# Kernel tuning notes

Measured on AMD Instinct MI355X. Metric: run time of the kernel, lower is better.

The kernel has to match this reference:

```python
import jax, jax.numpy as jnp
import numpy as np

I, O, H, M, N = 64, 64, 512, 64, 128  # input, output, controller hidden, content bits, addresses
B, S = 32, 256
EPS = 1e-8
R_SZ = M + 6          # read head: key(M) + beta(1) + gate(1) + shift(3) + gamma(1)
W_SZ = 3 * M + 6      # write head: read params + erase(M) + add(M)


def _split_head(p, with_erase_add):
    k = jnp.tanh(p[:, :M])
    beta = jax.nn.softplus(p[:, M:M + 1])
    g = jax.nn.sigmoid(p[:, M + 1:M + 2])
    s = jax.nn.softmax(p[:, M + 2:M + 5], axis=-1)
    gamma = 1.0 + jax.nn.softplus(p[:, M + 5:M + 6])
    if with_erase_add:
        e = jax.nn.sigmoid(p[:, M + 6:2 * M + 6])
        a = jnp.tanh(p[:, 2 * M + 6:3 * M + 6])
        return k, beta, g, s, gamma, e, a
    return k, beta, g, s, gamma


def _address(k, beta, g, s, gamma, w_prev, mem):
    # k:[B,M] beta,g,gamma:[B,1] s:[B,3] w_prev:[B,N] mem:[B,N,M]
    knorm = jnp.linalg.norm(k, axis=-1, keepdims=True)   # [B,1]
    mnorm = jnp.linalg.norm(mem, axis=-1)                # [B,N]
    sim = jnp.einsum('bm,bnm->bn', k, mem) / (knorm * mnorm + EPS)
    wc = jax.nn.softmax(beta * sim, axis=-1)             # content addressing
    wg = g * wc + (1.0 - g) * w_prev                     # interpolation gate
    # circular convolution with shifts {-1, 0, +1}
    rolled = jnp.stack([jnp.roll(wg, o, axis=-1) for o in (-1, 0, 1)], axis=-1)  # [B,N,3]
    ws = jnp.einsum('bnt,bt->bn', rolled, s)
    wp = jnp.power(jnp.maximum(ws, 1e-12), gamma)        # sharpening
    return wp / jnp.sum(wp, axis=-1, keepdims=True)


def setup_inputs() -> dict:
    key = jax.random.key(0)
    ks = jax.random.split(key, 5)
    sc = 0.05
    ctrl_in = I + M + H  # external input + read vector + recurrent hidden
    return {
        'inputs': jax.random.normal(ks[0], (B, S, I), jnp.float32),
        'W_lstm': jax.random.normal(ks[1], (ctrl_in, 4 * H), jnp.float32) * sc,
        'b_lstm': jnp.zeros((4 * H,), jnp.float32),
        'W_int': jax.random.normal(ks[2], (H, R_SZ + W_SZ), jnp.float32) * sc,
        'b_int': jnp.zeros((R_SZ + W_SZ,), jnp.float32),
        'W_out': jax.random.normal(ks[3], (H + M, O), jnp.float32) * sc,
        'b_out': jnp.zeros((O,), jnp.float32),
    }


def reference(inputs, W_lstm, b_lstm, W_int, b_int, W_out, b_out):
    Bsz = inputs.shape[0]
    mem0 = jnp.full((Bsz, N, M), 0.01, jnp.float32)
    w0 = jnp.zeros((Bsz, N), jnp.float32).at[:, 0].set(1.0)
    h0 = jnp.zeros((Bsz, H), jnp.float32)
    c0 = jnp.zeros((Bsz, H), jnp.float32)
    r0 = jnp.full((Bsz, M), 0.01, jnp.float32)

    def step(carry, x_t):
        h, c, w_r, w_w, mem, r = carry
        # LSTM controller over [input, read vector]
        z = jnp.concatenate([x_t, r, h], axis=-1) @ W_lstm + b_lstm
        i_g, f_g, g_g, o_g = jnp.split(z, 4, axis=-1)
        c = jax.nn.sigmoid(f_g) * c + jax.nn.sigmoid(i_g) * jnp.tanh(g_g)
        h = jax.nn.sigmoid(o_g) * jnp.tanh(c)
        # interface parameters
        p = h @ W_int + b_int
        rk, rb, rg, rs, rgam = _split_head(p[:, :R_SZ], False)
        wk, wb, wg_, ws_, wgam, e, a = _split_head(p[:, R_SZ:], True)
        # write (erase then add), then read from updated memory
        w_w = _address(wk, wb, wg_, ws_, wgam, w_w, mem)
        mem = mem * (1.0 - w_w[:, :, None] * e[:, None, :]) + w_w[:, :, None] * a[:, None, :]
        w_r = _address(rk, rb, rg, rs, rgam, w_r, mem)
        r = jnp.einsum('bn,bnm->bm', w_r, mem)
        out = jnp.concatenate([h, r], axis=-1) @ W_out + b_out
        return (h, c, w_r, w_w, mem, r), out

    xs = jnp.swapaxes(inputs, 0, 1)  # [S,B,I]
    _, outs = jax.lax.scan(step, (h0, c0, w0, w0, mem0, r0), xs)
    return jnp.swapaxes(outs, 0, 1)  # [B,S,O]
```

## Files before the change

kernel.cpp:

```cpp
#include <hip/hip_runtime.h>
#include <hip/hip_fp16.h>
#include <math.h>

#define NI 64
#define NO 64
#define NH 512
#define NM 64
#define NN 128
#define NB 32
#define NS 256
#define ZD 2048
#define PD 268
#define NG 128
#define GBLK 160
#define TPB 512
#define UPB 4
#define ST 580
#define RS_ST 68

__device__ __forceinline__ float fexp(float x){ return __expf(x); }
__device__ __forceinline__ float sigm(float x){ return 1.0f/(1.0f+__expf(-x)); }
__device__ __forceinline__ float ftanh(float x){
  float e = __expf(2.f*x);
  return (x > 10.f) ? 1.f : (x < -10.f) ? -1.f : (e - 1.f)/(e + 1.f);
}
__device__ __forceinline__ float softplus_(float x){
  return (x > 15.f) ? x : __logf(1.f + __expf(x));
}
__device__ __forceinline__ float fpow_(float x, float g){
  return __expf(g*__logf(x));
}

typedef _Float16 h2_t __attribute__((ext_vector_type(2)));
#if defined(__has_builtin)
#if __has_builtin(__builtin_amdgcn_fdot2)
#define HAS_FDOT2 1
#endif
#endif
__device__ __forceinline__ float fdot2_(unsigned int w, unsigned int h, float acc){
#ifdef HAS_FDOT2
  return __builtin_amdgcn_fdot2(__builtin_bit_cast(h2_t, w),
                                __builtin_bit_cast(h2_t, h), acc, false);
#else
  float w0 = __half2float(__builtin_bit_cast(__half, (unsigned short)(w      )));
  float w1 = __half2float(__builtin_bit_cast(__half, (unsigned short)(w >> 16)));
  float h0 = __half2float(__builtin_bit_cast(__half, (unsigned short)(h      )));
  float h1 = __half2float(__builtin_bit_cast(__half, (unsigned short)(h >> 16)));
  return fmaf(w1, h1, fmaf(w0, h0, acc));
#endif
}

__device__ __forceinline__ float cloadf(const float* p){
  return __hip_atomic_load(p, __ATOMIC_RELAXED, __HIP_MEMORY_SCOPE_SYSTEM);
}
__device__ __forceinline__ void cstoref(float* p, float v){
  __hip_atomic_store(p, v, __ATOMIC_RELAXED, __HIP_MEMORY_SCOPE_SYSTEM);
}
__device__ __forceinline__ float2 cloadf2(const float* p){
  unsigned long long u = __hip_atomic_load((const unsigned long long*)p,
                                           __ATOMIC_RELAXED, __HIP_MEMORY_SCOPE_SYSTEM);
  return __builtin_bit_cast(float2, u);
}
__device__ __forceinline__ unsigned long long cload8(const void* p){
  return __hip_atomic_load((const unsigned long long*)p,
                           __ATOMIC_RELAXED, __HIP_MEMORY_SCOPE_SYSTEM);
}
__device__ __forceinline__ void cstore8(void* p, unsigned long long v){
  __hip_atomic_store((unsigned long long*)p, v,
                     __ATOMIC_RELAXED, __HIP_MEMORY_SCOPE_SYSTEM);
}
__device__ __forceinline__ int cloadi(const int* p){
  return __hip_atomic_load(p, __ATOMIC_RELAXED, __HIP_MEMORY_SCOPE_SYSTEM);
}
__device__ __forceinline__ void cstorei(int* p, int v){
  __hip_atomic_store(p, v, __ATOMIC_RELAXED, __HIP_MEMORY_SCOPE_SYSTEM);
}
__device__ __forceinline__ void caddi(int* p){
  __hip_atomic_fetch_add(p, 1, __ATOMIC_RELAXED, __HIP_MEMORY_SCOPE_SYSTEM);
}
__device__ __forceinline__ void cstoreh(unsigned short* p, unsigned short v){
  __hip_atomic_store(p, v, __ATOMIC_RELAXED, __HIP_MEMORY_SCOPE_SYSTEM);
}

__device__ __forceinline__ unsigned long long packh4(float a, float b, float c, float d){
  unsigned short u0 = __builtin_bit_cast(unsigned short, __float2half(a));
  unsigned short u1 = __builtin_bit_cast(unsigned short, __float2half(b));
  unsigned short u2 = __builtin_bit_cast(unsigned short, __float2half(c));
  unsigned short u3 = __builtin_bit_cast(unsigned short, __float2half(d));
  return (unsigned long long)u0 | ((unsigned long long)u1 << 16)
       | ((unsigned long long)u2 << 32) | ((unsigned long long)u3 << 48);
}
__device__ __forceinline__ void unpackh4(unsigned long long v, float* o){
  o[0] = __half2float(__builtin_bit_cast(__half, (unsigned short)(v      )));
  o[1] = __half2float(__builtin_bit_cast(__half, (unsigned short)(v >> 16)));
  o[2] = __half2float(__builtin_bit_cast(__half, (unsigned short)(v >> 32)));
  o[3] = __half2float(__builtin_bit_cast(__half, (unsigned short)(v >> 48)));
}

__device__ __forceinline__ void postFlag(int* flags, int idx, int era){
  __syncthreads();
  if (threadIdx.x == 0) cstorei(&flags[idx*16], era);
}
__device__ __forceinline__ void waitAll32(const int* flags, int era){
  if (threadIdx.x < 32) {
    while (cloadi(&flags[(int)threadIdx.x*16]) < era)
      __builtin_amdgcn_s_sleep(1);
  }
  __syncthreads();
}
__device__ __forceinline__ void postCnt(int* c){
  __syncthreads();
  if (threadIdx.x == 0) caddi(c);
}
__device__ __forceinline__ void waitCnt(const int* c, int target){
  if (threadIdx.x == 0) {
    while (cloadi(c) < target) __builtin_amdgcn_s_sleep(2);
  }
  __syncthreads();
}

struct P1S { float inT[NB*ST]; float zpart[4*16*32]; float rs[NB*RS_ST]; float hx[4*33]; };
struct P3S { float h[NH]; unsigned long long h16[128]; float pp[544]; float p[PD+4];
             float rk[NM], wk[NM], e[NM], a[NM];
             float sim[NN]; float red[8*64]; float r[NM]; };
union  USH { P1S p1; P3S p3; };

__device__ void address_head(int t, const float* __restrict__ ks,
                             const float* __restrict__ scal,
                             float* __restrict__ w_arr,
                             const float* __restrict__ mem_s,
                             float* __restrict__ sim_s)
{
  {
    int n = t >> 2, sub = t & 3;
    int cn = (n & 7) << 2;
    float dot = 0.f, sq = 0.f;
#pragma unroll
    for (int i = 0; i < 16; i += 4) {
      int m = sub*16 + i;
      float4 mv = *(const float4*)&mem_s[n*NM + (m ^ cn)];
      float4 kv = *(const float4*)&ks[m];
      dot = fmaf(kv.x, mv.x, dot); dot = fmaf(kv.y, mv.y, dot);
      dot = fmaf(kv.z, mv.z, dot); dot = fmaf(kv.w, mv.w, dot);
      sq  = fmaf(mv.x, mv.x, sq);  sq  = fmaf(mv.y, mv.y, sq);
      sq  = fmaf(mv.z, mv.z, sq);  sq  = fmaf(mv.w, mv.w, sq);
    }
    dot += __shfl_xor(dot, 1); sq += __shfl_xor(sq, 1);
    dot += __shfl_xor(dot, 2); sq += __shfl_xor(sq, 2);
    if (sub == 0) sim_s[n] = dot / (scal[0]*sqrtf(sq) + 1e-8f);
  }
  __syncthreads();
  if (t < 64) {
    int l = t;
    float beta = scal[1], g = scal[2], s0 = scal[3], s1 = scal[4], s2 = scal[5], gamma = scal[6];
    float x0 = beta*sim_s[l], x1 = beta*sim_s[l+64];
    float mx = fmaxf(x0, x1);
#pragma unroll
    for (int off=32; off; off>>=1) mx = fmaxf(mx, __shfl_xor(mx, off));
    float e0 = fexp(x0-mx), e1 = fexp(x1-mx);
    float sm = e0+e1;
#pragma unroll
    for (int off=32; off; off>>=1) sm += __shfl_xor(sm, off);
    float inv = 1.0f/sm;
    float wg0 = g*e0*inv + (1.f-g)*w_arr[l];
    float wg1 = g*e1*inv + (1.f-g)*w_arr[l+64];
    float up0 = __shfl(wg0, (l+1)&63);
    float w1f = __shfl(wg1, 0);
    float plus0 = (l==63) ? w1f : up0;
    float dn0 = __shfl(wg0, (l-1)&63);
    float w1b = __shfl(wg1, 63);
    float minus0 = (l==0) ? w1b : dn0;
    float up1 = __shfl(wg1, (l+1)&63);
    float w0f = __shfl(wg0, 0);
    float plus1 = (l==63) ? w0f : up1;
    float dn1 = __shfl(wg1, (l-1)&63);
    float w0b = __shfl(wg0, 63);
    float minus1 = (l==0) ? w0b : dn1;
    float ws0 = s0*plus0 + s1*wg0 + s2*minus0;
    float ws1 = s0*plus1 + s1*wg1 + s2*minus1;
    float wp0 = fpow_(fmaxf(ws0, 1e-12f), gamma);
    float wp1 = fpow_(fmaxf(ws1, 1e-12f), gamma);
    float tot = wp0+wp1;
#pragma unroll
    for (int off=32; off; off>>=1) tot += __shfl_xor(tot, off);
    float invt = 1.0f/tot;
    w_arr[l]    = wp0*invt;
    w_arr[l+64] = wp1*invt;
  }
  __syncthreads();
}

extern "C" __global__ __launch_bounds__(TPB, 1)
void ntm_coop(const float* __restrict__ inputs, const float* __restrict__ W_lstm,
              const float* __restrict__ b_lstm, const float* __restrict__ W_int,
              const float* __restrict__ b_int, const float* __restrict__ W_out,
              const float* __restrict__ b_out, float* __restrict__ out,
              float* __restrict__ wsf)
{
  __shared__ float mem_s[NN*NM];
  __shared__ float wr_s[NN], ww_s[NN];
  __shared__ float scal_s[14];
  __shared__ USH u;

  int*    cbase   = (int*)wsf;
  int*    flags_r = (int*)wsf + 1024;
  __half* hT16    = (__half*)(wsf + 8192);
  float*  rT      = wsf + 8192 + 16384;
  float*  WrT     = rT + NB*NM;
  unsigned short* WintT16 = (unsigned short*)(WrT + ZD*64);
  unsigned short* WoutT16 = WintT16 + PD*NH;

  const int t   = threadIdx.x;
  const int bid = blockIdx.x;
  const bool isB = (bid < NB);

  {
    int gid = bid*TPB + t;
    for (int idx = gid; idx < PD*NH; idx += GBLK*TPB) {
      int c = idx >> 9, k = idx & 511;
      cstoreh(&WintT16[idx],
              __builtin_bit_cast(unsigned short, __float2half(W_int[(size_t)k*PD + c])));
    }
    for (int idx = gid; idx < NO*576; idx += GBLK*TPB) {
      int c = idx / 576, k = idx - c*576;
      cstoreh(&WoutT16[idx],
              __builtin_bit_cast(unsigned short, __float2half(W_out[(size_t)k*NO + c])));
    }
    for (int idx = gid; idx < ZD*64; idx += GBLK*TPB) {
      int c = idx >> 6, k = idx & 63;
      cstoref(&WrT[idx], W_lstm[(size_t)(64 + k)*ZD + c]);
    }
  }
  postCnt(&cbase[256]);
  waitCnt(&cbase[256], GBLK);

  if (!isB) {
    const int gb   = bid - NB;
    const int pb_  = t & 31;
    const int gate = (t >> 5) & 3;
    const int kp   = t >> 7;
    const int j0   = ((gb & 7) << 6) + ((gb >> 3) * UPB);
    const int colg = gate*NH + j0;
    const int pj   = t >> 5;
    const int pw   = t & 31;
    const int q_g  = gb & 7;
    float c_reg = 0.f;
    __syncthreads();

    for (int step = 0; step < NS; ++step) {
      const __half* h16_prev = hT16 + (size_t)((step & 1) ^ 1)*NH*NB;
      __half*       h16_cur  = hT16 + (size_t)(step & 1)*NH*NB;

      if (step) {
        if (t < 8) {
          const int tgt = 16*step;
          while (cloadi(&cbase[t*16]) < tgt) __builtin_amdgcn_s_sleep(1);
        }
        __syncthreads();
      }

      { int sb = t >> 4, k4 = (t & 15) * 4;
        float4 xv = *(const float4*)(inputs + ((size_t)sb*NS + step)*NI + k4);
        *(float4*)&u.p1.inT[sb*ST + k4] = xv; }
      if (step == 0) {
#pragma unroll
        for (int i = 0; i < 8; ++i) {
          int q = t + 512*i; int b_ = q >> 7, u_ = (q & 127) * 4;
          *(float4*)&u.p1.inT[b_*ST + 64 + u_] = make_float4(0.f,0.f,0.f,0.f);
        }
      } else {
#pragma unroll
        for (int i = 0; i < 8; ++i) {
          int q = t + 512*i; int b_ = q >> 7, u_ = (q & 127) * 4;
          unsigned long long v = cload8(h16_prev + b_*NH + u_);
          float o[4]; unpackh4(v, o);
          *(float4*)&u.p1.inT[b_*ST + 64 + u_] = make_float4(o[0],o[1],o[2],o[3]);
        }
      }
      __syncthreads();

      float a0=0.f, a1=0.f, a2=0.f, a3=0.f;
      {
        const float* xr = &u.p1.inT[pb_*ST + kp*16];
        const float* Wp = W_lstm + (size_t)(kp*16)*ZD + colg;
#pragma unroll
        for (int k4 = 0; k4 < 16; k4 += 4) {
          float4 x = *(const float4*)&xr[k4];
          float4 w0 = *(const float4*)(Wp + (size_t)(k4+0)*ZD);
          float4 w1 = *(const float4*)(Wp + (size_t)(k4+1)*ZD);
          float4 w2 = *(const float4*)(Wp + (size_t)(k4+2)*ZD);
          float4 w3 = *(const float4*)(Wp + (size_t)(k4+3)*ZD);
          a0 = fmaf(x.x, w0.x, a0); a1 = fmaf(x.x, w0.y, a1);
          a2 = fmaf(x.x, w0.z, a2); a3 = fmaf(x.x, w0.w, a3);
          a0 = fmaf(x.y, w1.x, a0); a1 = fmaf(x.y, w1.y, a1);
          a2 = fmaf(x.y, w1.z, a2); a3 = fmaf(x.y, w1.w, a3);
          a0 = fmaf(x.z, w2.x, a0); a1 = fmaf(x.z, w2.y, a1);
          a2 = fmaf(x.z, w2.z, a2); a3 = fmaf(x.z, w2.w, a3);
          a0 = fmaf(x.w, w3.x, a0); a1 = fmaf(x.w, w3.y, a1);
          a2 = fmaf(x.w, w3.z, a2); a3 = fmaf(x.w, w3.w, a3);
        }
        const float* hr = &u.p1.inT[pb_*ST + 64 + kp*128];
        const float* Wh = W_lstm + (size_t)(128 + kp*128)*ZD + colg;
#pragma unroll 4
        for (int k4 = 0; k4 < 128; k4 += 4) {
          float4 x = *(const float4*)&hr[k4];
          float4 w0 = *(const float4*)(Wh + (size_t)(k4+0)*ZD);
          float4 w1 = *(const float4*)(Wh + (size_t)(k4+1)*ZD);
          float4 w2 = *(const float4*)(Wh + (size_t)(k4+2)*ZD);
          float4 w3 = *(const float4*)(Wh + (size_t)(k4+3)*ZD);
          a0 = fmaf(x.x, w0.x, a0); a1 = fmaf(x.x, w0.y, a1);
          a2 = fmaf(x.x, w0.z, a2); a3 = fmaf(x.x, w0.w, a3);
          a0 = fmaf(x.y, w1.x, a0); a1 = fmaf(x.y, w1.y, a1);
          a2 = fmaf(x.y, w1.z, a2); a3 = fmaf(x.y, w1.w, a3);
          a0 = fmaf(x.z, w2.x, a0); a1 = fmaf(x.z, w2.y, a1);
          a2 = fmaf(x.z, w2.z, a2); a3 = fmaf(x.z, w2.w, a3);
          a0 = fmaf(x.w, w3.x, a0); a1 = fmaf(x.w, w3.y, a1);
          a2 = fmaf(x.w, w3.z, a2); a3 = fmaf(x.w, w3.w, a3);
        }
        if (step == 0) {
          const float* Wr0 = W_lstm + (size_t)(64 + kp*16)*ZD + colg;
#pragma unroll
          for (int k = 0; k < 16; ++k) {
            float4 w = *(const float4*)(Wr0 + (size_t)k*ZD);
            a0 = fmaf(0.01f, w.x, a0); a1 = fmaf(0.01f, w.y, a1);
            a2 = fmaf(0.01f, w.z, a2); a3 = fmaf(0.01f, w.w, a3);
          }
        }
      }
      { int base = (kp*16 + gate*4)*32 + pb_;
        u.p1.zpart[base]    = a0;
        u.p1.zpart[base+32] = a1;
        u.p1.zpart[base+64] = a2;
        u.p1.zpart[base+96] = a3; }

      if (step) {
        waitAll32(flags_r, step);
        { int e = 2*t; int bb = e >> 6, kk = e & 63;
          float2 v = cloadf2(rT + e);
          *(float2*)&u.p1.rs[bb*RS_ST + kk] = v;
          e += 1024; bb = e >> 6; kk = e & 63;
          v = cloadf2(rT + e);
          *(float2*)&u.p1.rs[bb*RS_ST + kk] = v; }
      }
      __syncthreads();

      if (t < 128) {
        float zrv[4] = {0.f, 0.f, 0.f, 0.f};
        if (step) {
          const float* rr = &u.p1.rs[pw*RS_ST];
#pragma unroll
          for (int gt = 0; gt < 4; ++gt) {
            const float* Wc = WrT + (size_t)(gt*NH + j0 + pj)*64;
            float acc = 0.f;
#pragma unroll
            for (int k = 0; k < 64; k += 4) {
              float4 w = *(const float4*)&Wc[k];
              acc = fmaf(rr[k],   w.x, acc);
              acc = fmaf(rr[k+1], w.y, acc);
              acc = fmaf(rr[k+2], w.z, acc);
              acc = fmaf(rr[k+3], w.w, acc);
            }
            zrv[gt] = acc;
          }
        }
        float zv[4];
#pragma unroll
        for (int gt = 0; gt < 4; ++gt) {
          int ci = gt*4 + pj;
          zv[gt] = u.p1.zpart[ci*32 + pw] + u.p1.zpart[(16+ci)*32 + pw]
                 + u.p1.zpart[(32+ci)*32 + pw] + u.p1.zpart[(48+ci)*32 + pw]
                 + zrv[gt] + b_lstm[gt*NH + j0 + pj];
        }
        float cn = sigm(zv[1])*c_reg + sigm(zv[0])*ftanh(zv[2]);
        c_reg = cn;
        u.p1.hx[pj*33 + pw] = sigm(zv[3])*ftanh(cn);
      }
      __syncthreads();
      if (t < 32) {
        unsigned long long v = packh4(u.p1.hx[t], u.p1.hx[33+t],
                                      u.p1.hx[66+t], u.p1.hx[99+t]);
        cstore8(h16_cur + t*NH + j0, v);
      }
      postCnt(&cbase[q_g*16]);
    }
  } else {
    const int b = bid;
    for (int i = t; i < NN*NM; i += TPB) mem_s[i] = 0.01f;
    if (t < NN) { wr_s[t] = (t==0)?1.f:0.f; ww_s[t] = (t==0)?1.f:0.f; }
    __syncthreads();

    for (int step = 0; step < NS; ++step) {
      const int era = step + 1;
      const __half* h16_cur = hT16 + (size_t)(step & 1)*NH*NB;

      if (t < 8) {
        const int tgt = 16*era;
        while (cloadi(&cbase[t*16]) < tgt) __builtin_amdgcn_s_sleep(1);
      }
      __syncthreads();

      if (t < 128) {
        unsigned long long v = cload8(h16_cur + b*NH + 4*t);
        u.p3.h16[t] = v;
        float o[4]; unpackh4(v, o);
        *(float4*)&u.p3.h[4*t] = make_float4(o[0],o[1],o[2],o[3]);
      }
      __syncthreads();

      {
        int c = t >> 1, kh = t & 1;
        const unsigned long long* Wc =
            (const unsigned long long*)(WintT16 + (size_t)c*512 + kh*256);
        const unsigned long long* hh = u.p3.h16 + kh*64;
        float pacc = 0.f;
#pragma unroll 8
        for (int k = 0; k < 64; ++k) {
          unsigned long long w = Wc[k], hv = hh[k];
          pacc = fdot2_((unsigned int)w,        (unsigned int)hv,        pacc);
          pacc = fdot2_((unsigned int)(w >> 32),(unsigned int)(hv >> 32), pacc);
        }
        u.p3.pp[t] = pacc;
        if (t < 24) {
          int id = 512 + t; int c2 = id >> 1; int k2 = id & 1;
          const unsigned long long* Wc2 =
              (const unsigned long long*)(WintT16 + (size_t)c2*512 + k2*256);
          const unsigned long long* hh2 = u.p3.h16 + k2*64;
          float pa2 = 0.f;
#pragma unroll 8
          for (int k = 0; k < 64; ++k) {
            unsigned long long w = Wc2[k], hv = hh2[k];
            pa2 = fdot2_((unsigned int)w,        (unsigned int)hv,        pa2);
            pa2 = fdot2_((unsigned int)(w >> 32),(unsigned int)(hv >> 32), pa2);
          }
          u.p3.pp[id] = pa2;
        }
      }
      __syncthreads();
      if (t < PD) u.p3.p[t] = u.p3.pp[2*t] + u.p3.pp[2*t+1] + b_int[t];
      __syncthreads();

      if (t < NM) {
        float rk = ftanh(u.p3.p[t]);
        float wk = ftanh(u.p3.p[70+t]);
        u.p3.rk[t] = rk; u.p3.wk[t] = wk;
        u.p3.e[t] = sigm(u.p3.p[140+t]);
        u.p3.a[t] = ftanh(u.p3.p[204+t]);
        float sr = rk*rk, sw = wk*wk;
#pragma unroll
        for (int off=32; off; off>>=1){ sr += __shfl_xor(sr,off); sw += __shfl_xor(sw,off); }
        if (t == 0) { scal_s[0] = sqrtf(sr); scal_s[7] = sqrtf(sw); }
      }
      if (t == 64) {
        scal_s[1] = softplus_(u.p3.p[64]);
        scal_s[2] = sigm(u.p3.p[65]);
        float a0=u.p3.p[66], a1=u.p3.p[67], a2=u.p3.p[68];
        float m = fmaxf(a0,fmaxf(a1,a2));
        float e0=fexp(a0-m), e1=fexp(a1-m), e2=fexp(a2-m);
        float s = e0+e1+e2;
        scal_s[3]=e0/s; scal_s[4]=e1/s; scal_s[5]=e2/s;
        scal_s[6] = 1.f + softplus_(u.p3.p[69]);
      }
      if (t == 128) {
        scal_s[8]  = softplus_(u.p3.p[134]);
        scal_s[9]  = sigm(u.p3.p[135]);
        float a0=u.p3.p[136], a1=u.p3.p[137], a2=u.p3.p[138];
        float m = fmaxf(a0,fmaxf(a1,a2));
        float e0=fexp(a0-m), e1=fexp(a1-m), e2=fexp(a2-m);
        float s = e0+e1+e2;
        scal_s[10]=e0/s; scal_s[11]=e1/s; scal_s[12]=e2/s;
        scal_s[13] = 1.f + softplus_(u.p3.p[139]);
      }
      __syncthreads();

      address_head(t, u.p3.wk, &scal_s[7], ww_s, mem_s, u.p3.sim);

      {
        int n = t >> 2, sub = t & 3;
        int cn = (n & 7) << 2;
        float w = ww_s[n];
#pragma unroll
        for (int i = 0; i < 16; i += 4) {
          int m = sub*16 + i;
          float* mp = &mem_s[n*NM + (m ^ cn)];
          float4 mv = *(float4*)mp;
          float4 ev = *(const float4*)&u.p3.e[m];
          float4 av = *(const float4*)&u.p3.a[m];
          mv.x = mv.x*(1.f - w*ev.x) + w*av.x;
          mv.y = mv.y*(1.f - w*ev.y) + w*av.y;
          mv.z = mv.z*(1.f - w*ev.z) + w*av.z;
          mv.w = mv.w*(1.f - w*ev.w) + w*av.w;
          *(float4*)mp = mv;
        }
      }
      __syncthreads();

      address_head(t, u.p3.rk, &scal_s[0], wr_s, mem_s, u.p3.sim);

      {
        int part = t >> 6, m = t & 63;
        float racc = 0.f;
#pragma unroll
        for (int nn = 0; nn < 16; ++nn) {
          int n = part*16 + nn;
          racc = fmaf(wr_s[n], mem_s[n*NM + (m ^ ((n&7)<<2))], racc);
        }
        u.p3.red[part*64 + m] = racc;
      }
      __syncthreads();
      if (t < NM) {
        float rv = 0.f;
#pragma unroll
        for (int pq = 0; pq < 8; ++pq) rv += u.p3.red[pq*64 + t];
        u.p3.r[t] = rv;
        cstoref(&rT[b*NM + t], rv);
      }
      postFlag(flags_r, b, era);

      {
        int part = t >> 6, c = t & 63;
        const unsigned long long* Wc =
            (const unsigned long long*)(WoutT16 + (size_t)c*576 + part*72);
        float oacc = 0.f;
        int k0 = part*72;
#pragma unroll
        for (int kk = 0; kk < 72; kk += 4) {
          float o[4]; unpackh4(Wc[kk >> 2], o);
          int k = k0 + kk;
          float v0 = (k   < NH) ? u.p3.h[k]   : u.p3.r[k-NH];
          float v1 = (k+1 < NH) ? u.p3.h[k+1] : u.p3.r[k+1-NH];
          float v2 = (k+2 < NH) ? u.p3.h[k+2] : u.p3.r[k+2-NH];
          float v3 = (k+3 < NH) ? u.p3.h[k+3] : u.p3.r[k+3-NH];
          oacc = fmaf(v0, o[0], oacc);
          oacc = fmaf(v1, o[1], oacc);
          oacc = fmaf(v2, o[2], oacc);
          oacc = fmaf(v3, o[3], oacc);
        }
        u.p3.red[part*64 + c] = oacc;
      }
      __syncthreads();
      if (t < NO) {
        float ov = b_out[t];
#pragma unroll
        for (int pq = 0; pq < 8; ++pq) ov += u.p3.red[pq*64 + t];
        out[(size_t)b*NS*NO + (size_t)step*NO + t] = ov;
      }
      __syncthreads();
    }
  }
}

extern "C" void kernel_launch(void* const* d_in, const int* in_sizes, int n_in,
                              void* d_out, int out_size, void* d_ws, size_t ws_size,
                              hipStream_t stream) {
  const float* inputs = (const float*)d_in[0];
  const float* W_lstm = (const float*)d_in[1];
  const float* b_lstm = (const float*)d_in[2];
  const float* W_int  = (const float*)d_in[3];
  const float* b_int  = (const float*)d_in[4];
  const float* W_out  = (const float*)d_in[5];
  const float* b_out  = (const float*)d_in[6];
  float* outp = (float*)d_out;
  float* wsp  = (float*)d_ws;

  hipMemsetAsync(d_ws, 0, 32768, stream);

  void* args[] = { (void*)&inputs, (void*)&W_lstm, (void*)&b_lstm,
                   (void*)&W_int, (void*)&b_int, (void*)&W_out, (void*)&b_out,
                   (void*)&outp, (void*)&wsp };
  hipLaunchCooperativeKernel((const void*)ntm_coop, dim3(GBLK), dim3(TPB),
                             args, 0, stream);
}
```

Before: 5.261 ms.

## Split LSTM gate blocks by batch groups to narrow inter-block synchronisation

```diff
diff --git a/kernel.cpp b/kernel.cpp
--- a/kernel.cpp
+++ b/kernel.cpp
@@ -14,7 +14,6 @@
 #define NG 128
 #define GBLK 160
 #define TPB 512
-#define UPB 4
 #define ST 580
 #define RS_ST 68
 
@@ -101,13 +100,6 @@
   __syncthreads();
   if (threadIdx.x == 0) cstorei(&flags[idx*16], era);
 }
-__device__ __forceinline__ void waitAll32(const int* flags, int era){
-  if (threadIdx.x < 32) {
-    while (cloadi(&flags[(int)threadIdx.x*16]) < era)
-      __builtin_amdgcn_s_sleep(1);
-  }
-  __syncthreads();
-}
 __device__ __forceinline__ void postCnt(int* c){
   __syncthreads();
   if (threadIdx.x == 0) caddi(c);
@@ -119,7 +111,8 @@
   __syncthreads();
 }
 
-struct P1S { float inT[NB*ST]; float zpart[4*16*32]; float rs[NB*RS_ST]; float hx[4*33]; };
+struct P1S { float inT[8*ST]; float zpart[64*36]; float zfull[512];
+             float rs[8*RS_ST]; float hx[16*9]; };
 struct P3S { float h[NH]; unsigned long long h16[128]; float pp[544]; float p[PD+4];
              float rk[NM], wk[NM], e[NM], a[NM];
              float sim[NN]; float red[8*64]; float r[NM]; };
@@ -236,14 +229,20 @@
 
   if (!isB) {
     const int gb   = bid - NB;
-    const int pb_  = t & 31;
-    const int gate = (t >> 5) & 3;
+    const int bg   = gb >> 5;
+    const int gbl  = gb & 31;
+    const int b0   = bg * 8;
+    const int j0   = ((gbl & 7) << 6) + ((gbl >> 3) << 4);
     const int kp   = t >> 7;
-    const int j0   = ((gb & 7) << 6) + ((gb >> 3) * UPB);
-    const int colg = gate*NH + j0;
-    const int pj   = t >> 5;
-    const int pw   = t & 31;
-    const int q_g  = gb & 7;
+    const int rem  = t & 127;
+    const int c4   = rem >> 3;
+    const int pb8  = rem & 7;
+    const int gate4= c4 >> 2;
+    const int u4   = (c4 & 3) * 4;
+    const int colg = gate4*NH + j0 + u4;
+    const int pj   = t >> 3;
+    const int pw8  = t & 7;
+    const int cntq = bg*2 + (gbl >> 4);
     float c_reg = 0.f;
     __syncthreads();
 
@@ -251,28 +250,31 @@
       const __half* h16_prev = hT16 + (size_t)((step & 1) ^ 1)*NH*NB;
       __half*       h16_cur  = hT16 + (size_t)(step & 1)*NH*NB;
 
+      if (t < 128) {
+        int sb = t >> 4, k4 = (t & 15) * 4;
+        float4 xv = *(const float4*)(inputs + ((size_t)(b0+sb)*NS + step)*NI + k4);
+        *(float4*)&u.p1.inT[sb*ST + k4] = xv;
+      }
+
       if (step) {
-        if (t < 8) {
+        if (t < 2) {
           const int tgt = 16*step;
-          while (cloadi(&cbase[t*16]) < tgt) __builtin_amdgcn_s_sleep(1);
+          while (cloadi(&cbase[(bg*2 + t)*16]) < tgt) __builtin_amdgcn_s_sleep(1);
         }
         __syncthreads();
       }
 
-      { int sb = t >> 4, k4 = (t & 15) * 4;
-        float4 xv = *(const float4*)(inputs + ((size_t)sb*NS + step)*NI + k4);
-        *(float4*)&u.p1.inT[sb*ST + k4] = xv; }
       if (step == 0) {
 #pragma unroll
-        for (int i = 0; i < 8; ++i) {
+        for (int i = 0; i < 2; ++i) {
           int q = t + 512*i; int b_ = q >> 7, u_ = (q & 127) * 4;
           *(float4*)&u.p1.inT[b_*ST + 64 + u_] = make_float4(0.f,0.f,0.f,0.f);
         }
       } else {
 #pragma unroll
-        for (int i = 0; i < 8; ++i) {
+        for (int i = 0; i < 2; ++i) {
           int q = t + 512*i; int b_ = q >> 7, u_ = (q & 127) * 4;
-          unsigned long long v = cload8(h16_prev + b_*NH + u_);
+          unsigned long long v = cload8(h16_prev + (size_t)(b0+b_)*NH + u_);
           float o[4]; unpackh4(v, o);
           *(float4*)&u.p1.inT[b_*ST + 64 + u_] = make_float4(o[0],o[1],o[2],o[3]);
         }
@@ -281,7 +283,7 @@
 
       float a0=0.f, a1=0.f, a2=0.f, a3=0.f;
       {
-        const float* xr = &u.p1.inT[pb_*ST + kp*16];
+        const float* xr = &u.p1.inT[pb8*ST + kp*16];
         const float* Wp = W_lstm + (size_t)(kp*16)*ZD + colg;
 #pragma unroll
         for (int k4 = 0; k4 < 16; k4 += 4) {
@@ -299,7 +301,7 @@
           a0 = fmaf(x.w, w3.x, a0); a1 = fmaf(x.w, w3.y, a1);
           a2 = fmaf(x.w, w3.z, a2); a3 = fmaf(x.w, w3.w, a3);
         }
-        const float* hr = &u.p1.inT[pb_*ST + 64 + kp*128];
+        const float* hr = &u.p1.inT[pb8*ST + 64 + kp*128];
         const float* Wh = W_lstm + (size_t)(128 + kp*128)*ZD + colg;
 #pragma unroll 4
         for (int k4 = 0; k4 < 128; k4 += 4) {
@@ -327,27 +329,41 @@
           }
         }
       }
-      { int base = (kp*16 + gate*4)*32 + pb_;
-        u.p1.zpart[base]    = a0;
-        u.p1.zpart[base+32] = a1;
-        u.p1.zpart[base+64] = a2;
-        u.p1.zpart[base+96] = a3; }
+      { int base = (kp*16 + c4)*36 + pb8;
+        u.p1.zpart[base]      = a0;
+        u.p1.zpart[base + 9]  = a1;
+        u.p1.zpart[base + 18] = a2;
+        u.p1.zpart[base + 27] = a3; }
 
       if (step) {
-        waitAll32(flags_r, step);
-        { int e = 2*t; int bb = e >> 6, kk = e & 63;
-          float2 v = cloadf2(rT + e);
+        if (t < 8) {
+          while (cloadi(&flags_r[(b0 + t)*16]) < step) __builtin_amdgcn_s_sleep(1);
+        }
+        __syncthreads();
+        if (t < 256) {
+          int bb = t >> 5, kk = (t & 31) * 2;
+          float2 v = cloadf2(rT + (size_t)(b0+bb)*64 + kk);
           *(float2*)&u.p1.rs[bb*RS_ST + kk] = v;
-          e += 1024; bb = e >> 6; kk = e & 63;
-          v = cloadf2(rT + e);
-          *(float2*)&u.p1.rs[bb*RS_ST + kk] = v; }
+        }
+      }
+      __syncthreads();
+
+      {
+        int col = t >> 3, pb = t & 7;
+        int c4r = col >> 2, cir = col & 3;
+        float z = u.p1.zpart[(c4r)*36 + cir*9 + pb]
+                + u.p1.zpart[(16 + c4r)*36 + cir*9 + pb]
+                + u.p1.zpart[(32 + c4r)*36 + cir*9 + pb]
+                + u.p1.zpart[(48 + c4r)*36 + cir*9 + pb]
+                + b_lstm[(col >> 4)*NH + j0 + (col & 15)];
+        u.p1.zfull[t] = z;
       }
       __syncthreads();
 
       if (t < 128) {
         float zrv[4] = {0.f, 0.f, 0.f, 0.f};
         if (step) {
-          const float* rr = &u.p1.rs[pw*RS_ST];
+          const float* rr = &u.p1.rs[pw8*RS_ST];
 #pragma unroll
           for (int gt = 0; gt < 4; ++gt) {
             const float* Wc = WrT + (size_t)(gt*NH + j0 + pj)*64;
@@ -365,26 +381,26 @@
         }
         float zv[4];
 #pragma unroll
-        for (int gt = 0; gt < 4; ++gt) {
-          int ci = gt*4 + pj;
-          zv[gt] = u.p1.zpart[ci*32 + pw] + u.p1.zpart[(16+ci)*32 + pw]
-                 + u.p1.zpart[(32+ci)*32 + pw] + u.p1.zpart[(48+ci)*32 + pw]
-                 + zrv[gt] + b_lstm[gt*NH + j0 + pj];
-        }
+        for (int gt = 0; gt < 4; ++gt)
+          zv[gt] = u.p1.zfull[(gt*16 + pj)*8 + pw8] + zrv[gt];
         float cn = sigm(zv[1])*c_reg + sigm(zv[0])*ftanh(zv[2]);
         c_reg = cn;
-        u.p1.hx[pj*33 + pw] = sigm(zv[3])*ftanh(cn);
+        u.p1.hx[pj*9 + pw8] = sigm(zv[3])*ftanh(cn);
       }
       __syncthreads();
       if (t < 32) {
-        unsigned long long v = packh4(u.p1.hx[t], u.p1.hx[33+t],
-                                      u.p1.hx[66+t], u.p1.hx[99+t]);
-        cstore8(h16_cur + t*NH + j0, v);
-      }
-      postCnt(&cbase[q_g*16]);
+        int b8 = t >> 2, q4 = t & 3;
+        unsigned long long v = packh4(u.p1.hx[(q4*4+0)*9 + b8],
+                                      u.p1.hx[(q4*4+1)*9 + b8],
+                                      u.p1.hx[(q4*4+2)*9 + b8],
+                                      u.p1.hx[(q4*4+3)*9 + b8]);
+        cstore8(h16_cur + (size_t)(b0+b8)*NH + j0 + q4*4, v);
+      }
+      postCnt(&cbase[cntq*16]);
     }
   } else {
     const int b = bid;
+    const int g = b >> 3;
     for (int i = t; i < NN*NM; i += TPB) mem_s[i] = 0.01f;
     if (t < NN) { wr_s[t] = (t==0)?1.f:0.f; ww_s[t] = (t==0)?1.f:0.f; }
     __syncthreads();
@@ -393,14 +409,14 @@
       const int era = step + 1;
       const __half* h16_cur = hT16 + (size_t)(step & 1)*NH*NB;
 
-      if (t < 8) {
+      if (t < 2) {
         const int tgt = 16*era;
-        while (cloadi(&cbase[t*16]) < tgt) __builtin_amdgcn_s_sleep(1);
+        while (cloadi(&cbase[(g*2 + t)*16]) < tgt) __builtin_amdgcn_s_sleep(1);
       }
       __syncthreads();
 
       if (t < 128) {
-        unsigned long long v = cload8(h16_cur + b*NH + 4*t);
+        unsigned long long v = cload8(h16_cur + (size_t)b*NH + 4*t);
         u.p3.h16[t] = v;
         float o[4]; unpackh4(v, o);
         *(float4*)&u.p3.h[4*t] = make_float4(o[0],o[1],o[2],o[3]);
```

After: 5.363 ms. No clear change (+1.9%).
